# Kernel optimization log

Hardware: AMD Instinct MI355X
Metric: run time of the kernel (lower is better)

Reference implementation:

```python
import jax, jax.numpy as jnp
import numpy as np

GRID_SIZE = 5
SPLINE_ORDER = 3
NUM_EXPERTS = 8
TOP_K = 2
CAP_FACTOR = 1.25
TEMP = 1.0
GDHW = (4, 4, 4)


def make_grid(in_features):
    # efficient-KAN grid buffer: grid_range=[-1,1], extended by spline_order on each side
    h = 2.0 / GRID_SIZE
    g = jnp.arange(-SPLINE_ORDER, GRID_SIZE + SPLINE_ORDER + 1, dtype=jnp.float32) * h - 1.0
    return jnp.broadcast_to(g, (in_features, g.shape[0]))


def b_splines(x, grid):
    # x: (N, in) -> (N, in, GRID_SIZE + SPLINE_ORDER) Cox-de Boor bases
    x = x[:, :, None]
    bases = ((x >= grid[:, :-1]) & (x < grid[:, 1:])).astype(x.dtype)
    for k in range(1, SPLINE_ORDER + 1):
        left = (x - grid[:, : -(k + 1)]) / (grid[:, k:-1] - grid[:, : -(k + 1)])
        right = (grid[:, k + 1:] - x) / (grid[:, k + 1:] - grid[:, 1:-k])
        bases = left * bases[:, :, :-1] + right * bases[:, :, 1:]
    return bases


def kan_linear(x, base_w, spline_w, scaler, grid):
    base = jax.nn.silu(x) @ base_w.T
    bs = b_splines(x, grid)                                   # (N, in, coef)
    spline = jnp.einsum('nic,oic->no', bs, spline_w * scaler[:, :, None])
    return base + spline


def layernorm(x, w, b, eps=1e-5):
    mu = x.mean(-1, keepdims=True)
    var = x.var(-1, keepdims=True)
    return (x - mu) / jnp.sqrt(var + eps) * w + b


def setup_inputs() -> dict:
    key = jax.random.key(0)
    ks = jax.random.split(key, 12)
    Cf, hidden, E, nc = 256, 170, NUM_EXPERTS, 2
    coef = GRID_SIZE + SPLINE_ORDER
    def nrm(k, shape, scale):
        return jax.random.normal(k, shape, dtype=jnp.float32) * scale
    return {
        'fpn_feat': nrm(ks[0], (8, 254, 32, 32, 32), 1.0),
        'seg_logits': nrm(ks[1], (8, 2, 32, 32, 32), 1.0),
        'ln_r_w': jnp.ones((Cf,), jnp.float32),
        'ln_r_b': jnp.zeros((Cf,), jnp.float32),
        'ln_h_w': jnp.ones((Cf,), jnp.float32),
        'ln_h_b': jnp.zeros((Cf,), jnp.float32),
        'router_w': nrm(ks[2], (E, Cf), Cf ** -0.5),
        'router_b': jnp.zeros((E,), jnp.float32),
        'bw1': nrm(ks[3], (E, hidden, Cf), Cf ** -0.5),
        'sw1': nrm(ks[4], (E, hidden, Cf, coef), 0.1 * Cf ** -0.5),
        'sc1': nrm(ks[5], (E, hidden, Cf), Cf ** -0.5),
        'bw2': nrm(ks[6], (E, Cf, hidden), hidden ** -0.5),
        'sw2': nrm(ks[7], (E, Cf, hidden, coef), 0.1 * hidden ** -0.5),
        'sc2': nrm(ks[8], (E, Cf, hidden), hidden ** -0.5),
        'cls_bw': nrm(ks[9], (nc, Cf), Cf ** -0.5),
        'cls_sw': nrm(ks[10], (nc, Cf, coef), 0.1 * Cf ** -0.5),
        'cls_sc': nrm(ks[11], (nc, Cf), Cf ** -0.5),
        'grid_cf': make_grid(Cf),
        'grid_hid': make_grid(hidden),
    }


def reference(fpn_feat, seg_logits, ln_r_w, ln_r_b, ln_h_w, ln_h_b,
              router_w, router_b, bw1, sw1, sc1, bw2, sw2, sc2,
              cls_bw, cls_sw, cls_sc, grid_cf, grid_hid):
    fused = jnp.concatenate([fpn_feat, seg_logits], axis=1)   # (B, Cf, D, H, W)
    B, C, D, H, W = fused.shape
    gd, gh, gw = GDHW
    dp, hp, wp = D // gd, H // gh, W // gw
    # split into gd*gh*gw blocks per sample
    blk = fused.reshape(B, C, gd, dp, gh, hp, gw, wp)
    blk = blk.transpose(0, 2, 4, 6, 1, 3, 5, 7).reshape(-1, C, dp, hp, wp)
    vec = blk.mean(axis=(2, 3, 4))                            # (N, Cf) global avg pool

    N = vec.shape[0]
    E = NUM_EXPERTS
    x_norm = layernorm(vec, ln_r_w, ln_r_b)
    scores = (x_norm @ router_w.T + router_b) / TEMP          # (N, E)
    top_val, top_idx = jax.lax.top_k(scores, TOP_K)
    top_w = jax.nn.softmax(top_val, axis=-1)
    capacity = int(CAP_FACTOR * N * TOP_K / E) + 1

    onehot = top_idx[None] == jnp.arange(E)[:, None, None]    # (E, N, K)
    sel = onehot.any(-1)                                      # (E, N)
    pos = jnp.cumsum(sel.astype(jnp.int32), axis=1)           # rank among selected (1-based)
    keep = sel & (pos <= capacity)                            # capacity drop = first-come order
    w = (top_w[None] * onehot.astype(top_w.dtype)).sum(-1)    # (E, N) combine weights

    def expert(bw1e, sw1e, sc1e, bw2e, sw2e, sc2e):
        h = kan_linear(x_norm, bw1e, sw1e, sc1e, grid_cf)
        h = jax.nn.gelu(h, approximate=False)                 # torch nn.GELU default (erf)
        return kan_linear(h, bw2e, sw2e, sc2e, grid_hid)

    y_all = jax.vmap(expert)(bw1, sw1, sc1, bw2, sw2, sc2)    # (E, N, Cf)
    out = jnp.einsum('en,enc->nc', keep.astype(vec.dtype) * w, y_all)

    conf = scores.max(-1)                                     # (N,)
    logits_blk = kan_linear(layernorm(out, ln_h_w, ln_h_b), cls_bw, cls_sw, cls_sc, grid_cf)
    P = gd * gh * gw
    weight = jax.nn.softmax(conf.reshape(B, P), axis=-1)[:, :, None]
    logits = (logits_blk.reshape(B, P, -1) * weight).sum(1)   # (B, num_classes)
    return logits
```

## Files before the change

kernel.cpp:

```cpp
#include <hip/hip_runtime.h>
#include <math.h>

#define CF 256
#define HID 170
#define NE 8
#define NTOK 512
#define K1 2304
#define K2P 1536
#define CAPACITY 161

typedef __bf16 bf16x8 __attribute__((ext_vector_type(8)));
typedef unsigned short u16x8 __attribute__((ext_vector_type(8)));
typedef float f32x4 __attribute__((ext_vector_type(4)));

__device__ __forceinline__ float silu_f(float x) { return x / (1.0f + expf(-x)); }
__device__ __forceinline__ float gelu_f(float x) {
    return 0.5f * x * (1.0f + erff(x * 0.70710678118654752f));
}

__device__ __forceinline__ unsigned short f2bf(float f) {
    unsigned int u = __float_as_uint(f);
    u = u + 0x7fffu + ((u >> 16) & 1u);
    return (unsigned short)(u >> 16);
}

__device__ __forceinline__ void bspline8(float x, float bs[8]) {
    float b[11];
#pragma unroll
    for (int j = 0; j < 11; ++j) {
        float g0 = (float)(j - 3) * 0.4f - 1.0f;
        float g1 = (float)(j - 2) * 0.4f - 1.0f;
        b[j] = (x >= g0 && x < g1) ? 1.0f : 0.0f;
    }
#pragma unroll
    for (int k = 1; k <= 3; ++k) {
        float inv = 2.5f / (float)k;
#pragma unroll
        for (int j = 0; j < 10 - (k - 1); ++j) {
            float gj   = (float)(j - 3) * 0.4f - 1.0f;
            float gjk1 = (float)(j - 2 + k) * 0.4f - 1.0f;
            b[j] = (x - gj) * inv * b[j] + (gjk1 - x) * inv * b[j + 1];
        }
    }
#pragma unroll
    for (int c = 0; c < 8; ++c) bs[c] = b[c];
}

__global__ __launch_bounds__(256) void mega_front_kernel(const float* __restrict__ fpn,
                                                         const float* __restrict__ seg,
                                                         const float* __restrict__ bw1,
                                                         const float* __restrict__ sw1,
                                                         const float* __restrict__ sc1,
                                                         const float* __restrict__ bw2,
                                                         const float* __restrict__ sw2,
                                                         const float* __restrict__ sc2,
                                                         float* __restrict__ vec,
                                                         unsigned short* __restrict__ W1,
                                                         unsigned short* __restrict__ W2,
                                                         float* __restrict__ out) {
    int id = blockIdx.x, tid = threadIdx.x;
    if (id == 2048 && tid < 16) out[tid] = 0.0f;
    if (id < 2048) {
        int c = id & 255, b = id >> 8;
        const float* src = (c < 254) ? fpn + (size_t)(b * 254 + c) * 32768
                                     : seg + (size_t)(b * 2 + (c - 254)) * 32768;
        const float4* s4 = (const float4*)src;
        float s[4] = {0.f, 0.f, 0.f, 0.f};
#pragma unroll
        for (int it = 0; it < 32; ++it) {
            float4 v = s4[it * 256 + tid];
            s[it >> 3] += v.x + v.y + v.z + v.w;
        }
        __shared__ float acc[64];
        if (tid < 64) acc[tid] = 0.0f;
        __syncthreads();
        int bh = tid >> 6, bw = (tid & 7) >> 1;
#pragma unroll
        for (int bd = 0; bd < 4; ++bd) atomicAdd(&acc[bd * 16 + bh * 4 + bw], s[bd]);
        __syncthreads();
        if (tid < 64) vec[(size_t)(b * 64 + tid) * CF + c] = acc[tid] * (1.0f / 512.0f);
    } else if (id < 2048 + NE * HID) {
        int r = id - 2048;
        int o = r % HID, e = r / HID, i = tid;
        size_t oi = (size_t)(e * HID + o) * CF + i;
        unsigned short* row = W1 + (size_t)(e * HID + o) * K1;
        row[i] = f2bf(bw1[oi]);
        float sc = sc1[oi];
        const float* sw = sw1 + oi * 8;
        u16x8 pk;
#pragma unroll
        for (int c = 0; c < 8; ++c) pk[c] = f2bf(sw[c] * sc);
        *(u16x8*)(row + CF + i * 8) = pk;
    } else {
        int r = id - (2048 + NE * HID);
        int o = r & 255, e = r >> 8, t = tid;
        unsigned short* row = W2 + (size_t)(e * CF + o) * K2P;
        if (t < HID) {
            size_t oi = (size_t)(e * CF + o) * HID + t;
            row[t] = f2bf(bw2[oi]);
            float sc = sc2[oi];
            const float* sw = sw2 + oi * 8;
            u16x8 pk;
#pragma unroll
            for (int c = 0; c < 8; ++c) pk[c] = f2bf(sw[c] * sc);
            *(u16x8*)(row + HID + t * 8) = pk;
        } else if (t < HID + 6) {
            row[HID * 9 + (t - HID)] = 0;
        }
    }
}

__global__ __launch_bounds__(256) void ln_score_a1_kernel(const float* __restrict__ vec,
                                                          const float* __restrict__ lnw,
                                                          const float* __restrict__ lnb,
                                                          const float* __restrict__ rw,
                                                          const float* __restrict__ rb,
                                                          float* __restrict__ scores,
                                                          unsigned short* __restrict__ A1,
                                                          unsigned short* __restrict__ A2) {
    int n = blockIdx.x, i = threadIdx.x;
    if (i < 48) {
        int e = i / 6, j = i - e * 6;
        A2[((size_t)e * NTOK + n) * K2P + HID * 9 + j] = 0;
    }
    float v = vec[(size_t)n * CF + i];
    float s1 = v, s2 = v * v;
#pragma unroll
    for (int off = 32; off > 0; off >>= 1) {
        s1 += __shfl_xor(s1, off);
        s2 += __shfl_xor(s2, off);
    }
    __shared__ float rs1[4], rs2[4];
    int lane = i & 63, wid = i >> 6;
    if (lane == 0) { rs1[wid] = s1; rs2[wid] = s2; }
    __syncthreads();
    float tot1 = rs1[0] + rs1[1] + rs1[2] + rs1[3];
    float tot2 = rs2[0] + rs2[1] + rs2[2] + rs2[3];
    float mu = tot1 * (1.0f / CF);
    float var = tot2 * (1.0f / CF) - mu * mu;
    float rsd = rsqrtf(var + 1e-5f);
    float xv = (v - mu) * rsd * lnw[i] + lnb[i];
    unsigned short* r = A1 + (size_t)n * K1;
    r[i] = f2bf(silu_f(xv));
    float bs[8]; bspline8(xv, bs);
    u16x8 pk;
#pragma unroll
    for (int c = 0; c < 8; ++c) pk[c] = f2bf(bs[c]);
    *(u16x8*)(r + CF + i * 8) = pk;
    float p[NE];
#pragma unroll
    for (int e = 0; e < NE; ++e) p[e] = xv * rw[e * CF + i];
#pragma unroll
    for (int off = 32; off > 0; off >>= 1)
#pragma unroll
        for (int e = 0; e < NE; ++e) p[e] += __shfl_xor(p[e], off);
    __shared__ float pacc[4][NE];
    if (lane == 0)
#pragma unroll
        for (int e = 0; e < NE; ++e) pacc[wid][e] = p[e];
    __syncthreads();
    if (i < NE)
        scores[n * NE + i] = pacc[0][i] + pacc[1][i] + pacc[2][i] + pacc[3][i] + rb[i];
}

template <int MODE>
__global__ __launch_bounds__(256) void gemm_mfma_kernel(
        const unsigned short* __restrict__ Ag, const unsigned short* __restrict__ Bg,
        float* __restrict__ C, unsigned short* __restrict__ A2,
        const float* __restrict__ scores, float* __restrict__ cw, float* __restrict__ conf,
        int N, int K, long sA, long sB, long sC, int ldc) {
    __shared__ alignas(16) unsigned char smem[65536];
    int tid = threadIdx.x;
    int lane = tid & 63, w = tid >> 6;

    if (MODE == 1 && blockIdx.x == 3) {
        if (blockIdx.y != 0 || blockIdx.z != 0) return;
        int* ti0 = (int*)smem;
        int* ti1 = ti0 + NTOK;
        float* tw0 = (float*)(ti1 + NTOK);
        float* tw1 = tw0 + NTOK;
#pragma unroll
        for (int half = 0; half < 2; ++half) {
            int t = half * 256 + tid;
            float m1 = -1e30f, m2 = -1e30f; int i1 = 0, i2 = 0;
#pragma unroll
            for (int e = 0; e < NE; ++e) {
                float sc = scores[t * NE + e];
                if (sc > m1) { m2 = m1; i2 = i1; m1 = sc; i1 = e; }
                else if (sc > m2) { m2 = sc; i2 = e; }
            }
            conf[t] = m1;
            float ew = expf(m2 - m1);
            ti0[t] = i1; ti1[t] = i2;
            tw0[t] = 1.0f / (1.0f + ew); tw1[t] = ew / (1.0f + ew);
        }
        __syncthreads();
#pragma unroll
        for (int e2 = 0; e2 < 2; ++e2) {
            int e = w * 2 + e2;
            int cnt = 0;
#pragma unroll
            for (int c = 0; c < NTOK / 64; ++c) {
                int t = c * 64 + lane;
                int h0 = (ti0[t] == e), h1 = (ti1[t] == e);
                int sel = h0 | h1;
                unsigned long long mask = __ballot(sel);
                int pos = cnt + (int)__popcll(mask & ((1ull << lane) - 1ull));
                float wv = 0.f;
                if (sel && pos < CAPACITY) wv = h0 ? tw0[t] : tw1[t];
                cw[e * NTOK + t] = wv;
                cnt += (int)__popcll(mask);
            }
        }
        return;
    }

    unsigned char* AsB = smem;
    unsigned char* BsB = smem + 32768;

    int e = blockIdx.z;
    const unsigned short* A = Ag + (size_t)e * sA;
    const unsigned short* B = Bg + (size_t)e * sB;
    int m0 = blockIdx.y * 64, n0 = blockIdx.x * 64;
    int wr = w >> 1, wc = w & 1;
    int fr = lane & 15, fg = lane >> 4;

    int r0 = tid >> 5, ch = tid & 31;
    int d0 = r0 * 512 + ((ch * 16) ^ ((r0 & 7) << 4));
    const unsigned short* aP = A + (size_t)(m0 + r0) * K + ch * 8;
    const unsigned short* bP = B + (size_t)(n0 + r0) * K + ch * 8;
    bool bOk[8];
#pragma unroll
    for (int q = 0; q < 8; ++q) bOk[q] = (n0 + r0 + q * 8) < N;
    const u16x8 zero8 = {0, 0, 0, 0, 0, 0, 0, 0};

    f32x4 acc[2][2];
#pragma unroll
    for (int i = 0; i < 2; ++i)
#pragma unroll
        for (int j = 0; j < 2; ++j)
#pragma unroll
            for (int r = 0; r < 4; ++r) acc[i][j][r] = 0.f;

    const int steps = K >> 8;
    u16x8 ra[8], rb[8];
#pragma unroll
    for (int q = 0; q < 8; ++q) {
        ra[q] = *(const u16x8*)(aP + (size_t)q * 8 * K);
        rb[q] = bOk[q] ? *(const u16x8*)(bP + (size_t)q * 8 * K) : zero8;
    }

    for (int s = 0; s < steps; ++s) {
        __syncthreads();
#pragma unroll
        for (int q = 0; q < 8; ++q) {
            *(u16x8*)(AsB + d0 + q * 4096) = ra[q];
            *(u16x8*)(BsB + d0 + q * 4096) = rb[q];
        }
        __syncthreads();
        if (s + 1 < steps) {
            int k0 = (s + 1) << 8;
#pragma unroll
            for (int q = 0; q < 8; ++q) {
                ra[q] = *(const u16x8*)(aP + (size_t)q * 8 * K + k0);
                rb[q] = bOk[q] ? *(const u16x8*)(bP + (size_t)q * 8 * K + k0) : zero8;
            }
        }
#pragma unroll
        for (int ks = 0; ks < 8; ++ks) {
            int kb = ks * 64 + fg * 16;
            u16x8 af[2], bf[2];
#pragma unroll
            for (int mf = 0; mf < 2; ++mf) {
                int row = wr * 32 + mf * 16 + fr;
                af[mf] = *(const u16x8*)(AsB + row * 512 + (kb ^ ((row & 7) << 4)));
            }
#pragma unroll
            for (int nf = 0; nf < 2; ++nf) {
                int row = wc * 32 + nf * 16 + fr;
                bf[nf] = *(const u16x8*)(BsB + row * 512 + (kb ^ ((row & 7) << 4)));
            }
#pragma unroll
            for (int mf = 0; mf < 2; ++mf)
#pragma unroll
                for (int nf = 0; nf < 2; ++nf)
                    acc[mf][nf] = __builtin_amdgcn_mfma_f32_16x16x32_bf16(
                        __builtin_bit_cast(bf16x8, af[mf]),
                        __builtin_bit_cast(bf16x8, bf[nf]), acc[mf][nf], 0, 0, 0);
        }
    }

    if (MODE == 1) {
#pragma unroll
        for (int mf = 0; mf < 2; ++mf)
#pragma unroll
            for (int nf = 0; nf < 2; ++nf)
#pragma unroll
                for (int r = 0; r < 4; ++r) {
                    int row = m0 + wr * 32 + mf * 16 + fg * 4 + r;
                    int col = n0 + wc * 32 + nf * 16 + fr;
                    if (col < N) {
                        float g = gelu_f(acc[mf][nf][r]);
                        unsigned short* rr = A2 + ((size_t)e * NTOK + row) * K2P;
                        rr[col] = f2bf(silu_f(g));
                        float bs[8]; bspline8(g, bs);
                        u16x8 pk;
#pragma unroll
                        for (int c = 0; c < 8; ++c) pk[c] = f2bf(bs[c]);
                        *(u16x8*)(rr + HID + col * 8) = pk;
                    }
                }
    } else {
        float* Ce = C + (size_t)e * sC;
#pragma unroll
        for (int mf = 0; mf < 2; ++mf)
#pragma unroll
            for (int nf = 0; nf < 2; ++nf)
#pragma unroll
                for (int r = 0; r < 4; ++r) {
                    int row = m0 + wr * 32 + mf * 16 + fg * 4 + r;
                    int col = n0 + wc * 32 + nf * 16 + fr;
                    if (col < N) Ce[(size_t)row * ldc + col] = acc[mf][nf][r];
                }
    }
}

__global__ __launch_bounds__(256) void combcls_kernel(const float* __restrict__ y,
                                                      const float* __restrict__ cw,
                                                      const float* __restrict__ conf,
                                                      const float* __restrict__ lnw,
                                                      const float* __restrict__ lnb,
                                                      const float* __restrict__ cbw,
                                                      const float* __restrict__ csw,
                                                      const float* __restrict__ csc,
                                                      float* __restrict__ out) {
    int n = blockIdx.x, i = threadIdx.x;
    float v = 0.f;
#pragma unroll
    for (int e = 0; e < NE; ++e)
        v += cw[e * NTOK + n] * y[((size_t)(e * NTOK + n)) * CF + i];
    float s1 = v, s2 = v * v;
#pragma unroll
    for (int off = 32; off > 0; off >>= 1) {
        s1 += __shfl_xor(s1, off);
        s2 += __shfl_xor(s2, off);
    }
    __shared__ float rA[4], rB[4], rP0[4], rP1[4];
    int lane = i & 63, wid = i >> 6;
    if (lane == 0) { rA[wid] = s1; rB[wid] = s2; }
    __syncthreads();
    float tot1 = rA[0] + rA[1] + rA[2] + rA[3];
    float tot2 = rB[0] + rB[1] + rB[2] + rB[3];
    float mu = tot1 * (1.0f / CF);
    float var = tot2 * (1.0f / CF) - mu * mu;
    float rs = rsqrtf(var + 1e-5f);
    float xh = (v - mu) * rs * lnw[i] + lnb[i];
    float si = silu_f(xh);
    float bs[8]; bspline8(xh, bs);
    float p0 = si * cbw[i], p1 = si * cbw[CF + i];
    float sp0 = 0.f, sp1 = 0.f;
#pragma unroll
    for (int c = 0; c < 8; ++c) {
        sp0 += bs[c] * csw[(size_t)i * 8 + c];
        sp1 += bs[c] * csw[(size_t)(CF + i) * 8 + c];
    }
    p0 += sp0 * csc[i];
    p1 += sp1 * csc[CF + i];
#pragma unroll
    for (int off = 32; off > 0; off >>= 1) {
        p0 += __shfl_xor(p0, off);
        p1 += __shfl_xor(p1, off);
    }
    if (lane == 0) { rP0[wid] = p0; rP1[wid] = p1; }
    __syncthreads();
    if (i < 64) {
        int b = n >> 6;
        float cf = conf[b * 64 + i];
        float mx = cf;
#pragma unroll
        for (int off = 32; off > 0; off >>= 1) mx = fmaxf(mx, __shfl_xor(mx, off));
        float ev = expf(cf - mx);
        float sum = ev;
#pragma unroll
        for (int off = 32; off > 0; off >>= 1) sum += __shfl_xor(sum, off);
        if (i == 0) {
            float wself = expf(conf[n] - mx) / sum;
            float l0 = rP0[0] + rP0[1] + rP0[2] + rP0[3];
            float l1 = rP1[0] + rP1[1] + rP1[2] + rP1[3];
            atomicAdd(&out[b * 2 + 0], wself * l0);
            atomicAdd(&out[b * 2 + 1], wself * l1);
        }
    }
}

extern "C" void kernel_launch(void* const* d_in, const int* in_sizes, int n_in,
                              void* d_out, int out_size, void* d_ws, size_t ws_size,
                              hipStream_t stream) {
    const float* fpn      = (const float*)d_in[0];
    const float* seg      = (const float*)d_in[1];
    const float* ln_r_w   = (const float*)d_in[2];
    const float* ln_r_b   = (const float*)d_in[3];
    const float* ln_h_w   = (const float*)d_in[4];
    const float* ln_h_b   = (const float*)d_in[5];
    const float* router_w = (const float*)d_in[6];
    const float* router_b = (const float*)d_in[7];
    const float* bw1      = (const float*)d_in[8];
    const float* sw1      = (const float*)d_in[9];
    const float* sc1      = (const float*)d_in[10];
    const float* bw2      = (const float*)d_in[11];
    const float* sw2      = (const float*)d_in[12];
    const float* sc2      = (const float*)d_in[13];
    const float* cls_bw   = (const float*)d_in[14];
    const float* cls_sw   = (const float*)d_in[15];
    const float* cls_sc   = (const float*)d_in[16];
    float* out = (float*)d_out;

    float* ws = (float*)d_ws;
    float* vec    = ws;
    float* scores = vec + 131072;
    float* cw     = scores + 4096;
    float* conf   = cw + 4096;
    float* yall   = conf + 512;
    unsigned short* A1b = (unsigned short*)(yall + 1048576);
    unsigned short* W1b = A1b + (size_t)NTOK * K1;
    unsigned short* A2b = W1b + (size_t)NE * HID * K1;
    unsigned short* W2b = A2b + (size_t)NE * NTOK * K2P;

    mega_front_kernel<<<dim3(2048 + NE * HID + 2048), dim3(256), 0, stream>>>(
        fpn, seg, bw1, sw1, sc1, bw2, sw2, sc2, vec, W1b, W2b, out);
    ln_score_a1_kernel<<<dim3(NTOK), dim3(256), 0, stream>>>(vec, ln_r_w, ln_r_b, router_w,
                                                             router_b, scores, A1b, A2b);
    gemm_mfma_kernel<1><<<dim3(4, 8, NE), dim3(256), 0, stream>>>(
        A1b, W1b, nullptr, A2b, scores, cw, conf, HID, K1, 0L, (long)HID * K1, 0L, 0);
    gemm_mfma_kernel<0><<<dim3(4, 8, NE), dim3(256), 0, stream>>>(
        A2b, W2b, yall, nullptr, nullptr, nullptr, nullptr, CF, K2P, (long)NTOK * K2P,
        (long)CF * K2P, (long)NTOK * CF, CF);
    combcls_kernel<<<dim3(NTOK), dim3(256), 0, stream>>>(yall, cw, conf, ln_h_w, ln_h_b,
                                                         cls_bw, cls_sw, cls_sc, out);
}
```

Baseline: 116.1 us.

## Fuse post-front stages into one persistent kernel with grid barriers

Replaces the four launches after the front kernel (LN/score, first GEMM plus routing, second GEMM, combine/classifier) with a single 256-block persistent kernel. The stages are separated by atomic-counter grid barriers whose counters are reset by the front kernel. The aim is to remove kernel launch gaps and tail effects between the small stages. In exchange it relies on all 256 blocks being co-resident, which the 64KB shared-memory footprint may limit, and it adds spin-wait barrier overhead.

```diff
diff --git a/kernel.cpp b/kernel.cpp
--- a/kernel.cpp
+++ b/kernel.cpp
@@ -8,6 +8,7 @@
 #define K1 2304
 #define K2P 1536
 #define CAPACITY 161
+#define NBLK 256
 
 typedef __bf16 bf16x8 __attribute__((ext_vector_type(8)));
 typedef unsigned short u16x8 __attribute__((ext_vector_type(8)));
@@ -57,9 +58,13 @@
                                                          float* __restrict__ vec,
                                                          unsigned short* __restrict__ W1,
                                                          unsigned short* __restrict__ W2,
+                                                         int* __restrict__ sync,
                                                          float* __restrict__ out) {
     int id = blockIdx.x, tid = threadIdx.x;
-    if (id == 2048 && tid < 16) out[tid] = 0.0f;
+    if (id == 2048) {
+        if (tid < 16) out[tid] = 0.0f;
+        if (tid >= 16 && tid < 32) sync[tid - 16] = 0;
+    }
     if (id < 2048) {
         int c = id & 255, b = id >> 8;
         const float* src = (c < 254) ? fpn + (size_t)(b * 254 + c) * 32768
@@ -110,118 +115,33 @@
     }
 }
 
-__global__ __launch_bounds__(256) void ln_score_a1_kernel(const float* __restrict__ vec,
-                                                          const float* __restrict__ lnw,
-                                                          const float* __restrict__ lnb,
-                                                          const float* __restrict__ rw,
-                                                          const float* __restrict__ rb,
-                                                          float* __restrict__ scores,
-                                                          unsigned short* __restrict__ A1,
-                                                          unsigned short* __restrict__ A2) {
-    int n = blockIdx.x, i = threadIdx.x;
-    if (i < 48) {
-        int e = i / 6, j = i - e * 6;
-        A2[((size_t)e * NTOK + n) * K2P + HID * 9 + j] = 0;
-    }
-    float v = vec[(size_t)n * CF + i];
-    float s1 = v, s2 = v * v;
-#pragma unroll
-    for (int off = 32; off > 0; off >>= 1) {
-        s1 += __shfl_xor(s1, off);
-        s2 += __shfl_xor(s2, off);
-    }
-    __shared__ float rs1[4], rs2[4];
-    int lane = i & 63, wid = i >> 6;
-    if (lane == 0) { rs1[wid] = s1; rs2[wid] = s2; }
+__device__ __forceinline__ void gridbar(int* cnt, int* flag, int tid) {
     __syncthreads();
-    float tot1 = rs1[0] + rs1[1] + rs1[2] + rs1[3];
-    float tot2 = rs2[0] + rs2[1] + rs2[2] + rs2[3];
-    float mu = tot1 * (1.0f / CF);
-    float var = tot2 * (1.0f / CF) - mu * mu;
-    float rsd = rsqrtf(var + 1e-5f);
-    float xv = (v - mu) * rsd * lnw[i] + lnb[i];
-    unsigned short* r = A1 + (size_t)n * K1;
-    r[i] = f2bf(silu_f(xv));
-    float bs[8]; bspline8(xv, bs);
-    u16x8 pk;
-#pragma unroll
-    for (int c = 0; c < 8; ++c) pk[c] = f2bf(bs[c]);
-    *(u16x8*)(r + CF + i * 8) = pk;
-    float p[NE];
-#pragma unroll
-    for (int e = 0; e < NE; ++e) p[e] = xv * rw[e * CF + i];
-#pragma unroll
-    for (int off = 32; off > 0; off >>= 1)
-#pragma unroll
-        for (int e = 0; e < NE; ++e) p[e] += __shfl_xor(p[e], off);
-    __shared__ float pacc[4][NE];
-    if (lane == 0)
-#pragma unroll
-        for (int e = 0; e < NE; ++e) pacc[wid][e] = p[e];
+    if (tid == 0) {
+        __threadfence();
+        if (atomicAdd(cnt, 1) == NBLK - 1) {
+            atomicExch(flag, 1);
+        } else {
+            while (atomicAdd(flag, 0) == 0) __builtin_amdgcn_s_sleep(2);
+        }
+        __threadfence();
+    }
     __syncthreads();
-    if (i < NE)
-        scores[n * NE + i] = pacc[0][i] + pacc[1][i] + pacc[2][i] + pacc[3][i] + rb[i];
 }
 
 template <int MODE>
-__global__ __launch_bounds__(256) void gemm_mfma_kernel(
-        const unsigned short* __restrict__ Ag, const unsigned short* __restrict__ Bg,
-        float* __restrict__ C, unsigned short* __restrict__ A2,
-        const float* __restrict__ scores, float* __restrict__ cw, float* __restrict__ conf,
-        int N, int K, long sA, long sB, long sC, int ldc) {
-    __shared__ alignas(16) unsigned char smem[65536];
-    int tid = threadIdx.x;
-    int lane = tid & 63, w = tid >> 6;
-
-    if (MODE == 1 && blockIdx.x == 3) {
-        if (blockIdx.y != 0 || blockIdx.z != 0) return;
-        int* ti0 = (int*)smem;
-        int* ti1 = ti0 + NTOK;
-        float* tw0 = (float*)(ti1 + NTOK);
-        float* tw1 = tw0 + NTOK;
-#pragma unroll
-        for (int half = 0; half < 2; ++half) {
-            int t = half * 256 + tid;
-            float m1 = -1e30f, m2 = -1e30f; int i1 = 0, i2 = 0;
-#pragma unroll
-            for (int e = 0; e < NE; ++e) {
-                float sc = scores[t * NE + e];
-                if (sc > m1) { m2 = m1; i2 = i1; m1 = sc; i1 = e; }
-                else if (sc > m2) { m2 = sc; i2 = e; }
-            }
-            conf[t] = m1;
-            float ew = expf(m2 - m1);
-            ti0[t] = i1; ti1[t] = i2;
-            tw0[t] = 1.0f / (1.0f + ew); tw1[t] = ew / (1.0f + ew);
-        }
-        __syncthreads();
-#pragma unroll
-        for (int e2 = 0; e2 < 2; ++e2) {
-            int e = w * 2 + e2;
-            int cnt = 0;
-#pragma unroll
-            for (int c = 0; c < NTOK / 64; ++c) {
-                int t = c * 64 + lane;
-                int h0 = (ti0[t] == e), h1 = (ti1[t] == e);
-                int sel = h0 | h1;
-                unsigned long long mask = __ballot(sel);
-                int pos = cnt + (int)__popcll(mask & ((1ull << lane) - 1ull));
-                float wv = 0.f;
-                if (sel && pos < CAPACITY) wv = h0 ? tw0[t] : tw1[t];
-                cw[e * NTOK + t] = wv;
-                cnt += (int)__popcll(mask);
-            }
-        }
-        return;
-    }
-
+__device__ __forceinline__ void gemm_tile(unsigned char* smem, int tid, int m0, int n0,
+                                          int e, const unsigned short* __restrict__ Ag,
+                                          const unsigned short* __restrict__ Bg,
+                                          float* __restrict__ C,
+                                          unsigned short* __restrict__ A2,
+                                          int N, int K, long sA, long sB, long sC,
+                                          int ldc) {
     unsigned char* AsB = smem;
     unsigned char* BsB = smem + 32768;
-
-    int e = blockIdx.z;
     const unsigned short* A = Ag + (size_t)e * sA;
     const unsigned short* B = Bg + (size_t)e * sB;
-    int m0 = blockIdx.y * 64, n0 = blockIdx.x * 64;
+    int lane = tid & 63, w = tid >> 6;
     int wr = w >> 1, wc = w & 1;
     int fr = lane & 15, fg = lane >> 4;
 
@@ -325,70 +245,182 @@
     }
 }
 
-__global__ __launch_bounds__(256) void combcls_kernel(const float* __restrict__ y,
-                                                      const float* __restrict__ cw,
-                                                      const float* __restrict__ conf,
-                                                      const float* __restrict__ lnw,
-                                                      const float* __restrict__ lnb,
-                                                      const float* __restrict__ cbw,
-                                                      const float* __restrict__ csw,
-                                                      const float* __restrict__ csc,
-                                                      float* __restrict__ out) {
-    int n = blockIdx.x, i = threadIdx.x;
-    float v = 0.f;
-#pragma unroll
-    for (int e = 0; e < NE; ++e)
-        v += cw[e * NTOK + n] * y[((size_t)(e * NTOK + n)) * CF + i];
-    float s1 = v, s2 = v * v;
-#pragma unroll
-    for (int off = 32; off > 0; off >>= 1) {
-        s1 += __shfl_xor(s1, off);
-        s2 += __shfl_xor(s2, off);
-    }
-    __shared__ float rA[4], rB[4], rP0[4], rP1[4];
+struct PArgs {
+    const float *vec, *lnr_w, *lnr_b, *lnh_w, *lnh_b, *rw, *rb, *cbw, *csw, *csc;
+    float *scores, *cw, *conf, *yall, *out;
+    unsigned short *A1, *W1, *A2, *W2;
+    int* sync;
+};
+
+__global__ __launch_bounds__(256) void moe_persist_kernel(PArgs a) {
+    __shared__ alignas(16) unsigned char smem[65536];
+    int bid = blockIdx.x, i = threadIdx.x;
     int lane = i & 63, wid = i >> 6;
-    if (lane == 0) { rA[wid] = s1; rB[wid] = s2; }
-    __syncthreads();
-    float tot1 = rA[0] + rA[1] + rA[2] + rA[3];
-    float tot2 = rB[0] + rB[1] + rB[2] + rB[3];
-    float mu = tot1 * (1.0f / CF);
-    float var = tot2 * (1.0f / CF) - mu * mu;
-    float rs = rsqrtf(var + 1e-5f);
-    float xh = (v - mu) * rs * lnw[i] + lnb[i];
-    float si = silu_f(xh);
-    float bs[8]; bspline8(xh, bs);
-    float p0 = si * cbw[i], p1 = si * cbw[CF + i];
-    float sp0 = 0.f, sp1 = 0.f;
-#pragma unroll
-    for (int c = 0; c < 8; ++c) {
-        sp0 += bs[c] * csw[(size_t)i * 8 + c];
-        sp1 += bs[c] * csw[(size_t)(CF + i) * 8 + c];
-    }
-    p0 += sp0 * csc[i];
-    p1 += sp1 * csc[CF + i];
-#pragma unroll
-    for (int off = 32; off > 0; off >>= 1) {
-        p0 += __shfl_xor(p0, off);
-        p1 += __shfl_xor(p1, off);
-    }
-    if (lane == 0) { rP0[wid] = p0; rP1[wid] = p1; }
-    __syncthreads();
-    if (i < 64) {
-        int b = n >> 6;
-        float cf = conf[b * 64 + i];
-        float mx = cf;
-#pragma unroll
-        for (int off = 32; off > 0; off >>= 1) mx = fmaxf(mx, __shfl_xor(mx, off));
-        float ev = expf(cf - mx);
-        float sum = ev;
-#pragma unroll
-        for (int off = 32; off > 0; off >>= 1) sum += __shfl_xor(sum, off);
-        if (i == 0) {
-            float wself = expf(conf[n] - mx) / sum;
-            float l0 = rP0[0] + rP0[1] + rP0[2] + rP0[3];
-            float l1 = rP1[0] + rP1[1] + rP1[2] + rP1[3];
-            atomicAdd(&out[b * 2 + 0], wself * l0);
-            atomicAdd(&out[b * 2 + 1], wself * l1);
+
+    {
+        float* shf = (float*)smem;
+#pragma unroll
+        for (int half = 0; half < 2; ++half) {
+            int n = bid * 2 + half;
+            if (i < 48) {
+                int e = i / 6, j = i - e * 6;
+                a.A2[((size_t)e * NTOK + n) * K2P + HID * 9 + j] = 0;
+            }
+            float v = a.vec[(size_t)n * CF + i];
+            float s1 = v, s2 = v * v;
+#pragma unroll
+            for (int off = 32; off > 0; off >>= 1) {
+                s1 += __shfl_xor(s1, off);
+                s2 += __shfl_xor(s2, off);
+            }
+            if (lane == 0) { shf[wid] = s1; shf[4 + wid] = s2; }
+            __syncthreads();
+            float tot1 = shf[0] + shf[1] + shf[2] + shf[3];
+            float tot2 = shf[4] + shf[5] + shf[6] + shf[7];
+            float mu = tot1 * (1.0f / CF);
+            float var = tot2 * (1.0f / CF) - mu * mu;
+            float rsd = rsqrtf(var + 1e-5f);
+            float xv = (v - mu) * rsd * a.lnr_w[i] + a.lnr_b[i];
+            unsigned short* r = a.A1 + (size_t)n * K1;
+            r[i] = f2bf(silu_f(xv));
+            float bs[8]; bspline8(xv, bs);
+            u16x8 pk;
+#pragma unroll
+            for (int c = 0; c < 8; ++c) pk[c] = f2bf(bs[c]);
+            *(u16x8*)(r + CF + i * 8) = pk;
+            float p[NE];
+#pragma unroll
+            for (int e = 0; e < NE; ++e) p[e] = xv * a.rw[e * CF + i];
+#pragma unroll
+            for (int off = 32; off > 0; off >>= 1)
+#pragma unroll
+                for (int e = 0; e < NE; ++e) p[e] += __shfl_xor(p[e], off);
+            if (lane == 0)
+#pragma unroll
+                for (int e = 0; e < NE; ++e) shf[8 + wid * NE + e] = p[e];
+            __syncthreads();
+            if (i < NE)
+                a.scores[n * NE + i] = shf[8 + i] + shf[8 + NE + i] +
+                                       shf[8 + 2 * NE + i] + shf[8 + 3 * NE + i] + a.rb[i];
+            __syncthreads();
+        }
+    }
+    gridbar(a.sync + 0, a.sync + 1, i);
+
+    if (bid < 192) {
+        int e = bid / 24, rem = bid % 24;
+        int m0 = (rem / 3) * 64, n0 = (rem % 3) * 64;
+        gemm_tile<1>(smem, i, m0, n0, e, a.A1, a.W1, nullptr, a.A2,
+                     HID, K1, 0L, (long)HID * K1, 0L, 0);
+    } else if (bid == 192) {
+        int* ti0 = (int*)smem;
+        int* ti1 = ti0 + NTOK;
+        float* tw0 = (float*)(ti1 + NTOK);
+        float* tw1 = tw0 + NTOK;
+#pragma unroll
+        for (int half = 0; half < 2; ++half) {
+            int t = half * 256 + i;
+            float m1 = -1e30f, m2 = -1e30f; int i1 = 0, i2 = 0;
+#pragma unroll
+            for (int e = 0; e < NE; ++e) {
+                float sc = a.scores[t * NE + e];
+                if (sc > m1) { m2 = m1; i2 = i1; m1 = sc; i1 = e; }
+                else if (sc > m2) { m2 = sc; i2 = e; }
+            }
+            a.conf[t] = m1;
+            float ew = expf(m2 - m1);
+            ti0[t] = i1; ti1[t] = i2;
+            tw0[t] = 1.0f / (1.0f + ew); tw1[t] = ew / (1.0f + ew);
+        }
+        __syncthreads();
+#pragma unroll
+        for (int e2 = 0; e2 < 2; ++e2) {
+            int e = wid * 2 + e2;
+            int cnt = 0;
+#pragma unroll
+            for (int c = 0; c < NTOK / 64; ++c) {
+                int t = c * 64 + lane;
+                int h0 = (ti0[t] == e), h1 = (ti1[t] == e);
+                int sel = h0 | h1;
+                unsigned long long mask = __ballot(sel);
+                int pos = cnt + (int)__popcll(mask & ((1ull << lane) - 1ull));
+                float wv = 0.f;
+                if (sel && pos < CAPACITY) wv = h0 ? tw0[t] : tw1[t];
+                a.cw[e * NTOK + t] = wv;
+                cnt += (int)__popcll(mask);
+            }
+        }
+    }
+    gridbar(a.sync + 2, a.sync + 3, i);
+
+    {
+        int e = bid >> 5, rem = bid & 31;
+        int m0 = (rem >> 2) * 64, n0 = (rem & 3) * 64;
+        gemm_tile<0>(smem, i, m0, n0, e, a.A2, a.W2, a.yall, nullptr,
+                     CF, K2P, (long)NTOK * K2P, (long)CF * K2P, (long)NTOK * CF, CF);
+    }
+    gridbar(a.sync + 4, a.sync + 5, i);
+
+    {
+        float* shf = (float*)smem;
+#pragma unroll
+        for (int half = 0; half < 2; ++half) {
+            int n = bid * 2 + half;
+            float v = 0.f;
+#pragma unroll
+            for (int e = 0; e < NE; ++e)
+                v += a.cw[e * NTOK + n] * a.yall[((size_t)(e * NTOK + n)) * CF + i];
+            float s1 = v, s2 = v * v;
+#pragma unroll
+            for (int off = 32; off > 0; off >>= 1) {
+                s1 += __shfl_xor(s1, off);
+                s2 += __shfl_xor(s2, off);
+            }
+            if (lane == 0) { shf[wid] = s1; shf[4 + wid] = s2; }
+            __syncthreads();
+            float tot1 = shf[0] + shf[1] + shf[2] + shf[3];
+            float tot2 = shf[4] + shf[5] + shf[6] + shf[7];
+            float mu = tot1 * (1.0f / CF);
+            float var = tot2 * (1.0f / CF) - mu * mu;
+            float rs = rsqrtf(var + 1e-5f);
+            float xh = (v - mu) * rs * a.lnh_w[i] + a.lnh_b[i];
+            float si = silu_f(xh);
+            float bs[8]; bspline8(xh, bs);
+            float p0 = si * a.cbw[i], p1 = si * a.cbw[CF + i];
+            float sp0 = 0.f, sp1 = 0.f;
+#pragma unroll
+            for (int c = 0; c < 8; ++c) {
+                sp0 += bs[c] * a.csw[(size_t)i * 8 + c];
+                sp1 += bs[c] * a.csw[(size_t)(CF + i) * 8 + c];
+            }
+            p0 += sp0 * a.csc[i];
+            p1 += sp1 * a.csc[CF + i];
+#pragma unroll
+            for (int off = 32; off > 0; off >>= 1) {
+                p0 += __shfl_xor(p0, off);
+                p1 += __shfl_xor(p1, off);
+            }
+            if (lane == 0) { shf[8 + wid] = p0; shf[12 + wid] = p1; }
+            __syncthreads();
+            if (i < 64) {
+                int b = n >> 6;
+                float cf = a.conf[b * 64 + i];
+                float mx = cf;
+#pragma unroll
+                for (int off = 32; off > 0; off >>= 1) mx = fmaxf(mx, __shfl_xor(mx, off));
+                float ev = expf(cf - mx);
+                float sum = ev;
+#pragma unroll
+                for (int off = 32; off > 0; off >>= 1) sum += __shfl_xor(sum, off);
+                if (i == 0) {
+                    float wself = expf(a.conf[n] - mx) / sum;
+                    float l0 = shf[8] + shf[9] + shf[10] + shf[11];
+                    float l1 = shf[12] + shf[13] + shf[14] + shf[15];
+                    atomicAdd(&a.out[b * 2 + 0], wself * l0);
+                    atomicAdd(&a.out[b * 2 + 1], wself * l1);
+                }
+            }
+            __syncthreads();
         }
     }
 }
@@ -420,21 +452,20 @@
     float* scores = vec + 131072;
     float* cw     = scores + 4096;
     float* conf   = cw + 4096;
-    float* yall   = conf + 512;
+    int*   syncb  = (int*)(conf + 512);
+    float* yall   = (float*)(syncb + 16);
     unsigned short* A1b = (unsigned short*)(yall + 1048576);
     unsigned short* W1b = A1b + (size_t)NTOK * K1;
     unsigned short* A2b = W1b + (size_t)NE * HID * K1;
     unsigned short* W2b = A2b + (size_t)NE * NTOK * K2P;
 
     mega_front_kernel<<<dim3(2048 + NE * HID + 2048), dim3(256), 0, stream>>>(
-        fpn, seg, bw1, sw1, sc1, bw2, sw2, sc2, vec, W1b, W2b, out);
-    ln_score_a1_kernel<<<dim3(NTOK), dim3(256), 0, stream>>>(vec, ln_r_w, ln_r_b, router_w,
-                                                             router_b, scores, A1b, A2b);
-    gemm_mfma_kernel<1><<<dim3(4, 8, NE), dim3(256), 0, stream>>>(
-        A1b, W1b, nullptr, A2b, scores, cw, conf, HID, K1, 0L, (long)HID * K1, 0L, 0);
-    gemm_mfma_kernel<0><<<dim3(4, 8, NE), dim3(256), 0, stream>>>(
-        A2b, W2b, yall, nullptr, nullptr, nullptr, nullptr, CF, K2P, (long)NTOK * K2P,
-        (long)CF * K2P, (long)NTOK * CF, CF);
-    combcls_kernel<<<dim3(NTOK), dim3(256), 0, stream>>>(yall, cw, conf, ln_h_w, ln_h_b,
-                                                         cls_bw, cls_sw, cls_sc, out);
-}
+        fpn, seg, bw1, sw1, sc1, bw2, sw2, sc2, vec, W1b, W2b, syncb, out);
+
+    PArgs a;
+    a.vec = vec; a.lnr_w = ln_r_w; a.lnr_b = ln_r_b; a.lnh_w = ln_h_w; a.lnh_b = ln_h_b;
+    a.rw = router_w; a.rb = router_b; a.cbw = cls_bw; a.csw = cls_sw; a.csc = cls_sc;
+    a.scores = scores; a.cw = cw; a.conf = conf; a.yall = yall; a.out = out;
+    a.A1 = A1b; a.W1 = W1b; a.A2 = A2b; a.W2 = W2b; a.sync = syncb;
+    moe_persist_kernel<<<dim3(NBLK), dim3(256), 0, stream>>>(a);
+}
```

After: 173.9 us. 1.5x slower.
